# Optimization experiments

Measured on AMD Instinct MI355X. Metric: run time of the kernel, lower is better.

Reference implementation:

```python
import jax, jax.numpy as jnp
import numpy as np
from jax import lax
from jax.scipy.special import logsumexp

B, S, T = 64, 512, 32
END_IND = T - 1  # module-level global in the original repo; bind to last tag


def setup_inputs() -> dict:
    key = jax.random.key(0)
    k1, k2, k3 = jax.random.split(key, 3)
    scores = jax.random.normal(k1, (B, S, T, T), dtype=jnp.float32)
    targets = jax.random.randint(k2, (B, S), 0, T * T, dtype=jnp.int32).astype(jnp.int64)
    # lengths in [1, S], sorted descending (pack_padded_sequence assumption)
    lengths = jnp.sort(jax.random.randint(k3, (B,), 1, S + 1, dtype=jnp.int32))[::-1]
    return {"scores": scores, "targets": targets, "lengths": lengths}


def reference(scores, targets, lengths):
    Bs, Ss, Ts, _ = scores.shape
    # gold score: gather flattened tag-pair score at each valid timestep
    flat = scores.reshape(Bs, Ss, Ts * Ts)
    gathered = jnp.take_along_axis(flat, targets[..., None], axis=2)[..., 0]  # [B,S]
    time_mask = jnp.arange(Ss)[None, :] < lengths[:, None]  # [B,S]
    gold_score = jnp.sum(jnp.where(time_mask, gathered, 0.0))

    # forward algorithm: fs[b, cur_tag], recurrence lse over prev_tag
    fs0 = logsumexp(scores[:, 0], axis=2)  # [B,T]
    sc_rest = jnp.swapaxes(scores, 0, 1)[1:]  # [S-1, B, T, T]
    active = jnp.arange(1, Ss)[:, None] < lengths[None, :]  # [S-1, B]

    def step(fs, xs):
        sc_t, act = xs  # [B,T,T], [B]
        new = logsumexp(sc_t + fs[:, None, :], axis=2)  # [B,T]
        return jnp.where(act[:, None], new, fs), None

    fs, _ = lax.scan(step, fs0, (sc_rest, active))
    all_scores = jnp.sum(fs[:, END_IND])
    return all_scores - gold_score
```

## Files before the change

### kernel.cpp

```cpp
#include <hip/hip_runtime.h>
#include <hip/hip_bf16.h>

#define BB 64
#define SS 512
#define TT 32
#define ENDI 31
#define NSEG 32
#define SEGLEN 16
#define ACCS 0
#define CNTS 1
#define GOLDB 16

typedef __attribute__((ext_vector_type(8))) short s8v;
typedef __attribute__((ext_vector_type(16))) float fx16;

union S8U {
  s8v v;
  unsigned int u[4];
};

__device__ __forceinline__ unsigned int cvtpk_bf16(float a, float b) {
  unsigned int r;
  asm("v_cvt_pk_bf16_f32 %0, %1, %2" : "=v"(r) : "v"(a), "v"(b));
  return r;
}

__global__ __launch_bounds__(64) void seg_kernel(
    const float* __restrict__ sc, const int* __restrict__ targets,
    const int* __restrict__ lengths, float* __restrict__ ws) {
  const int b = blockIdx.x;
  const int seg = blockIdx.y;
  const int l = threadIdx.x;
  const int c = l & 31;
  const int h = l >> 5;
  const int len = lengths[b];
  const int lo = seg * SEGLEN;

  if (b == 0 && seg == 0 && l == 0) {
    ws[ACCS] = 0.0f;
    ((unsigned*)ws)[CNTS] = 0u;
  }

  {
    float gv = 0.f;
    if (l < SEGLEN) {
      int s = lo + l;
      if (s < len) {
        int idx = b * SS + s;
        gv = sc[(size_t)idx * 1024 + (size_t)targets[idx]];
      }
    }
#pragma unroll
    for (int o = 32; o; o >>= 1) gv += __shfl_xor(gv, o);
    if (l == 0) ws[GOLDB + b * NSEG + seg] = gv;
  }

  float* mout = ws + GOLDB + BB * NSEG + (size_t)(b * NSEG + seg) * 1056;

  if (len <= lo) {
#pragma unroll
    for (int r = 0; r < 16; ++r) {
      int row = (r & 3) + 8 * (r >> 2) + 4 * h;
      mout[row * 32 + c] = (row == c) ? 1.0f : 0.0f;
    }
    if (l == 0) mout[1024] = 0.0f;
    return;
  }

  const int nsteps = (len - lo < SEGLEN) ? (len - lo) : SEGLEN;
  const float* base = sc + ((size_t)b * SS + lo) * 1024;

  S8U B0, B1;
#pragma unroll
  for (int q = 0; q < 4; ++q) {
    B0.u[q] = 0u;
    B1.u[q] = 0u;
  }
  {
    int j0 = c - 8 * h;
    if (j0 >= 0 && j0 < 8) B0.u[j0 >> 1] |= 0x3F80u << (16 * (j0 & 1));
    int j1 = c - 16 - 8 * h;
    if (j1 >= 0 && j1 < 8) B1.u[j1 >> 1] |= 0x3F80u << (16 * (j1 & 1));
  }

#define LOADE(buf, T)                                                     \
  do {                                                                    \
    const float* _p = base + (size_t)(T) * 1024 + c * 32 + 8 * h;         \
    float4 _a = *(const float4*)_p;                                       \
    float4 _b = *(const float4*)(_p + 4);                                 \
    float4 _c = *(const float4*)(_p + 16);                                \
    float4 _d = *(const float4*)(_p + 20);                                \
    buf[0] = _a.x;  buf[1] = _a.y;  buf[2] = _a.z;  buf[3] = _a.w;        \
    buf[4] = _b.x;  buf[5] = _b.y;  buf[6] = _b.z;  buf[7] = _b.w;        \
    buf[8] = _c.x;  buf[9] = _c.y;  buf[10] = _c.z; buf[11] = _c.w;       \
    buf[12] = _d.x; buf[13] = _d.y; buf[14] = _d.z; buf[15] = _d.w;       \
  } while (0)

#define RESCALE(SVAR)                                                     \
  do {                                                                    \
    float _mx = Cl[0];                                                    \
    _Pragma("unroll") for (int q = 1; q < 16; ++q) _mx = fmaxf(_mx, Cl[q]); \
    _mx = fmaxf(_mx, __shfl_xor(_mx, 32));                                \
    _mx = fmaxf(_mx, __shfl_xor(_mx, 1));                                 \
    _mx = fmaxf(_mx, __shfl_xor(_mx, 2));                                 \
    _mx = fmaxf(_mx, __shfl_xor(_mx, 4));                                 \
    _mx = fmaxf(_mx, __shfl_xor(_mx, 8));                                 \
    _mx = fmaxf(_mx, __shfl_xor(_mx, 16));                                \
    int _ex = ((__float_as_int(_mx) >> 23) & 255) - 127;                  \
    SVAR = __int_as_float((unsigned)(127 - _ex) << 23);                   \
    esum += _ex;                                                          \
  } while (0)

#define REPACK()                                                          \
  do {                                                                    \
    unsigned int W[8], X[8];                                              \
    _Pragma("unroll") for (int q = 0; q < 8; ++q) W[q] =                  \
        cvtpk_bf16(Cl[2 * q] * s, Cl[2 * q + 1] * s);                     \
    _Pragma("unroll") for (int q = 0; q < 8; ++q) X[q] =                  \
        __shfl_xor((int)W[q], 32);                                        \
    B0.u[0] = h ? X[2] : W[0];                                            \
    B0.u[1] = h ? X[3] : W[1];                                            \
    B0.u[2] = h ? W[2] : X[0];                                            \
    B0.u[3] = h ? W[3] : X[1];                                            \
    B1.u[0] = h ? X[6] : W[4];                                            \
    B1.u[1] = h ? X[7] : W[5];                                            \
    B1.u[2] = h ? W[6] : X[4];                                            \
    B1.u[3] = h ? W[7] : X[5];                                            \
  } while (0)

  int esum = 0;
  fx16 C;
#pragma unroll
  for (int q = 0; q < 16; ++q) C[q] = 0.f;

  if (nsteps == SEGLEN) {
    float L[4][16];
    S8U A4[4][2];
#pragma unroll
    for (int j = 0; j < 4; ++j) LOADE(L[j], j);

#pragma unroll
    for (int ch = 0; ch < 4; ++ch) {
#pragma unroll
      for (int k = 0; k < 4; ++k) {
#pragma unroll
        for (int q = 0; q < 4; ++q) {
          A4[k][0].u[q] =
              cvtpk_bf16(__expf(L[k][2 * q]), __expf(L[k][2 * q + 1]));
          A4[k][1].u[q] =
              cvtpk_bf16(__expf(L[k][8 + 2 * q]), __expf(L[k][9 + 2 * q]));
        }
      }
      if (ch < 3) {
#pragma unroll
        for (int j = 0; j < 4; ++j) LOADE(L[j], (ch + 1) * 4 + j);
      }
#pragma unroll
      for (int k = 0; k < 4; ++k) {
        fx16 Cl;
#pragma unroll
        for (int q = 0; q < 16; ++q) Cl[q] = 0.f;
        Cl = __builtin_amdgcn_mfma_f32_32x32x16_bf16(A4[k][0].v, B0.v, Cl,
                                                     0, 0, 0);
        Cl = __builtin_amdgcn_mfma_f32_32x32x16_bf16(A4[k][1].v, B1.v, Cl,
                                                     0, 0, 0);
        if (ch == 3 && k == 3) {
          C = Cl;
        } else {
          float s = 1.0f;
          if (k == 3) RESCALE(s);
          REPACK();
        }
      }
    }
  } else {
    float r0[16], r1[16], r2[16];
    LOADE(r0, 0);
    LOADE(r1, (nsteps > 1) ? 1 : 0);
    LOADE(r2, (nsteps > 2) ? 2 : 0);

#define STEPB(RB)                                                            \
    do {                                                                    \
      S8U A0, A1;                                                           \
      _Pragma("unroll") for (int q = 0; q < 4; ++q) {                       \
        A0.u[q] = cvtpk_bf16(__expf(RB[2 * q]), __expf(RB[2 * q + 1]));     \
        A1.u[q] = cvtpk_bf16(__expf(RB[8 + 2 * q]), __expf(RB[9 + 2 * q])); \
      }                                                                     \
      int _pf = t + 3;                                                      \
      if (_pf >= nsteps) _pf = nsteps - 1;                                  \
      LOADE(RB, _pf);                                                       \
      fx16 Cl;                                                              \
      _Pragma("unroll") for (int q = 0; q < 16; ++q) Cl[q] = 0.f;           \
      Cl = __builtin_amdgcn_mfma_f32_32x32x16_bf16(A0.v, B0.v, Cl, 0, 0, 0);\
      Cl = __builtin_amdgcn_mfma_f32_32x32x16_bf16(A1.v, B1.v, Cl, 0, 0, 0);\
      if (t + 1 < nsteps) {                                                 \
        float s = 1.0f;                                                     \
        if ((t & 3) == 3) RESCALE(s);                                       \
        REPACK();                                                           \
      } else {                                                              \
        C = Cl;                                                             \
      }                                                                     \
    } while (0)

    int t = 0;
    while (t < nsteps) {
      STEPB(r0);
      ++t;
      if (t >= nsteps) break;
      STEPB(r1);
      ++t;
      if (t >= nsteps) break;
      STEPB(r2);
      ++t;
    }
#undef STEPB
  }

  float mx = C[0];
#pragma unroll
  for (int q = 1; q < 16; ++q) mx = fmaxf(mx, C[q]);
  mx = fmaxf(mx, __shfl_xor(mx, 32));
  mx = fmaxf(mx, __shfl_xor(mx, 1));
  mx = fmaxf(mx, __shfl_xor(mx, 2));
  mx = fmaxf(mx, __shfl_xor(mx, 4));
  mx = fmaxf(mx, __shfl_xor(mx, 8));
  mx = fmaxf(mx, __shfl_xor(mx, 16));
  int ex = ((__float_as_int(mx) >> 23) & 255) - 127;
  float s = __int_as_float((unsigned)(127 - ex) << 23);
  esum += ex;
#pragma unroll
  for (int r = 0; r < 16; ++r) {
    int row = (r & 3) + 8 * (r >> 2) + 4 * h;
    mout[row * 32 + c] = C[r] * s;
  }
  if (l == 0) mout[1024] = (float)esum;
#undef REPACK
#undef RESCALE
#undef LOADE
}

__global__ __launch_bounds__(128) void comb_fin_kernel(
    float* __restrict__ ws, float* __restrict__ out) {
  const int b = blockIdx.x;
  const int w = threadIdx.x >> 6;
  const int l = threadIdx.x & 63;
  const int lo = l & 31;
  const int h = l >> 5;
  const int half = NSEG >> 1;
  __shared__ alignas(16) float st[2][TT];
  __shared__ float esvS[2];

#define FENCE() asm volatile("s_waitcnt lgkmcnt(0)" ::: "memory")

  float cur = w ? ((lo == ENDI) ? 1.0f : 0.0f) : 1.0f;
  st[w][lo] = cur;
  FENCE();

  const float* segbase = ws + GOLDB + BB * NSEG;
  float esv = 0.f;

#define LOADM(buf, SEG)                                                     \
  do {                                                                      \
    const float* _m = segbase + (size_t)(b * NSEG + (SEG)) * 1056;          \
    if (w == 0) {                        \
      const float4* _p = (const float4*)(_m + lo * 32 + h * 16);            \
      float4 _a = _p[0], _b2 = _p[1], _c2 = _p[2], _d = _p[3];              \
      buf[0] = _a.x;  buf[1] = _a.y;  buf[2] = _a.z;  buf[3] = _a.w;        \
      buf[4] = _b2.x; buf[5] = _b2.y; buf[6] = _b2.z; buf[7] = _b2.w;       \
      buf[8] = _c2.x; buf[9] = _c2.y; buf[10] = _c2.z; buf[11] = _c2.w;     \
      buf[12] = _d.x; buf[13] = _d.y; buf[14] = _d.z; buf[15] = _d.w;       \
    } else {      \
      const float* _p = _m + (h * 16) * 32 + lo;                            \
      _Pragma("unroll") for (int _j = 0; _j < 16; ++_j)                     \
          buf[_j] = _p[_j * 32];                                            \
    }                                                                       \
  } while (0)

  float mc[16], mn[16];
#pragma unroll
  for (int q = 0; q < 16; ++q) mn[q] = 0.f;
  {
    int seg0 = w ? (NSEG - 1) : 0;
    LOADM(mc, seg0);
  }
  for (int k = 0; k < half; ++k) {
    int segn = w ? (NSEG - 2 - k) : (k + 1);
    if (k + 1 < half) LOADM(mn, segn);
    int segc = w ? (NSEG - 1 - k) : k;
    esv += segbase[(size_t)(b * NSEG + segc) * 1056 + 1024];
    const float4* g4 = (const float4*)st[w];
    float4 g0 = g4[h * 4 + 0], g1 = g4[h * 4 + 1], g2 = g4[h * 4 + 2],
           g3 = g4[h * 4 + 3];
    float g[16] = {g0.x, g0.y, g0.z, g0.w, g1.x, g1.y, g1.z, g1.w,
                   g2.x, g2.y, g2.z, g2.w, g3.x, g3.y, g3.z, g3.w};
    float acc[4];
#pragma unroll
    for (int q = 0; q < 4; ++q) {
      acc[q] = mc[4 * q] * g[4 * q];
#pragma unroll
      for (int t = 1; t < 4; ++t)
        acc[q] = fmaf(mc[4 * q + t], g[4 * q + t], acc[q]);
    }
    float part = (acc[0] + acc[1]) + (acc[2] + acc[3]);
    cur = part + __shfl_xor(part, 32);
    if ((k & 3) == 3) {
      float mxv = cur;
      mxv = fmaxf(mxv, __shfl_xor(mxv, 1));
      mxv = fmaxf(mxv, __shfl_xor(mxv, 2));
      mxv = fmaxf(mxv, __shfl_xor(mxv, 4));
      mxv = fmaxf(mxv, __shfl_xor(mxv, 8));
      mxv = fmaxf(mxv, __shfl_xor(mxv, 16));
      int exv = ((__float_as_int(mxv) >> 23) & 255) - 127;
      cur *= __int_as_float((unsigned)(127 - exv) << 23);
      esv += (float)exv;
    }
    FENCE();
    st[w][lo] = cur;
    FENCE();
#pragma unroll
    for (int q = 0; q < 16; ++q) mc[q] = mn[q];
  }

  if (l == 0) esvS[w] = esv;
  __syncthreads();

  if (w == 0) {
    float pr = st[0][lo] * st[1][lo];
    float gd = ws[GOLDB + b * NSEG + lo];
#pragma unroll
    for (int o = 16; o; o >>= 1) {
      pr += __shfl_xor(pr, o);
      gd += __shfl_xor(gd, o);
    }
    if (l == 0) {
      float loss =
          (esvS[0] + esvS[1]) * 0.6931471805599453f + __logf(pr) - gd;
      atomicAdd(&ws[ACCS], loss);
      __threadfence();
      unsigned old = atomicAdd(&((unsigned*)ws)[CNTS], 1u);
      if (old == BB - 1) {
        float v = atomicAdd(&ws[ACCS], 0.0f);
        out[0] = v;
      }
    }
  }
#undef LOADM
#undef FENCE
}

extern "C" void kernel_launch(void* const* d_in, const int* in_sizes, int n_in,
                              void* d_out, int out_size, void* d_ws,
                              size_t ws_size, hipStream_t stream) {
  const float* scores = (const float*)d_in[0];
  const int* targets = (const int*)d_in[1];
  const int* lengths = (const int*)d_in[2];
  float* out = (float*)d_out;
  float* ws = (float*)d_ws;

  seg_kernel<<<dim3(BB, NSEG), 64, 0, stream>>>(scores, targets, lengths, ws);
  comb_fin_kernel<<<BB, 128, 0, stream>>>(ws, out);
}
```

Before: 49.79 us.

## Split each segment's chain across two waves and merge via LDS matmul

Each seg_kernel block now runs two wavefronts, and each one computes the product chain for half of a 16-step segment (8 steps each). The second wave normalizes its partial matrix and writes it to shared memory. The first wave then multiplies it in with one extra MFMA pair before writing out. This shortens the serial dependency chain per block and doubles the wave count, at the cost of a __syncthreads, LDS traffic, and one extra bf16 rounding in the merge.

```diff
diff --git a/kernel.cpp b/kernel.cpp
--- a/kernel.cpp
+++ b/kernel.cpp
@@ -7,6 +7,7 @@
 #define ENDI 31
 #define NSEG 32
 #define SEGLEN 16
+#define HALF 8
 #define ACCS 0
 #define CNTS 1
 #define GOLDB 16
@@ -25,23 +26,28 @@
   return r;
 }
 
-__global__ __launch_bounds__(64) void seg_kernel(
+__global__ __launch_bounds__(128) void seg_kernel(
     const float* __restrict__ sc, const int* __restrict__ targets,
     const int* __restrict__ lengths, float* __restrict__ ws) {
   const int b = blockIdx.x;
   const int seg = blockIdx.y;
-  const int l = threadIdx.x;
+  const int tid = threadIdx.x;
+  const int wv = tid >> 6;
+  const int l = tid & 63;
   const int c = l & 31;
   const int h = l >> 5;
   const int len = lengths[b];
   const int lo = seg * SEGLEN;
 
-  if (b == 0 && seg == 0 && l == 0) {
+  __shared__ alignas(16) float lm[TT * 33];
+  __shared__ float meta0;
+
+  if (b == 0 && seg == 0 && tid == 0) {
     ws[ACCS] = 0.0f;
     ((unsigned*)ws)[CNTS] = 0u;
   }
 
-  {
+  if (wv == 0) {
     float gv = 0.f;
     if (l < SEGLEN) {
       int s = lo + l;
@@ -58,17 +64,23 @@
   float* mout = ws + GOLDB + BB * NSEG + (size_t)(b * NSEG + seg) * 1056;
 
   if (len <= lo) {
-#pragma unroll
-    for (int r = 0; r < 16; ++r) {
-      int row = (r & 3) + 8 * (r >> 2) + 4 * h;
-      mout[row * 32 + c] = (row == c) ? 1.0f : 0.0f;
-    }
-    if (l == 0) mout[1024] = 0.0f;
+    if (wv == 0) {
+#pragma unroll
+      for (int r = 0; r < 16; ++r) {
+        int row = (r & 3) + 8 * (r >> 2) + 4 * h;
+        mout[row * 32 + c] = (row == c) ? 1.0f : 0.0f;
+      }
+      if (l == 0) mout[1024] = 0.0f;
+    }
     return;
   }
 
-  const int nsteps = (len - lo < SEGLEN) ? (len - lo) : SEGLEN;
-  const float* base = sc + ((size_t)b * SS + lo) * 1024;
+  const int rel = len - lo;
+  const int nst = (wv == 0) ? (rel < HALF ? rel : HALF)
+                            : (rel - HALF < 0 ? 0
+                                              : (rel - HALF < HALF ? rel - HALF
+                                                                   : HALF));
+  const float* base = sc + ((size_t)b * SS + lo + wv * HALF) * 1024;
 
   S8U B0, B1;
 #pragma unroll
@@ -133,51 +145,51 @@
 #pragma unroll
   for (int q = 0; q < 16; ++q) C[q] = 0.f;
 
-  if (nsteps == SEGLEN) {
-    float L[4][16];
-    S8U A4[4][2];
-#pragma unroll
-    for (int j = 0; j < 4; ++j) LOADE(L[j], j);
-
-#pragma unroll
-    for (int ch = 0; ch < 4; ++ch) {
-#pragma unroll
-      for (int k = 0; k < 4; ++k) {
+  if (nst == HALF) {
+    float L[2][16];
+    S8U A2[2][2];
+    LOADE(L[0], 0);
+    LOADE(L[1], 1);
+#pragma unroll
+    for (int ph = 0; ph < 4; ++ph) {
+#pragma unroll
+      for (int k = 0; k < 2; ++k) {
 #pragma unroll
         for (int q = 0; q < 4; ++q) {
-          A4[k][0].u[q] =
+          A2[k][0].u[q] =
               cvtpk_bf16(__expf(L[k][2 * q]), __expf(L[k][2 * q + 1]));
-          A4[k][1].u[q] =
+          A2[k][1].u[q] =
               cvtpk_bf16(__expf(L[k][8 + 2 * q]), __expf(L[k][9 + 2 * q]));
         }
       }
-      if (ch < 3) {
-#pragma unroll
-        for (int j = 0; j < 4; ++j) LOADE(L[j], (ch + 1) * 4 + j);
-      }
-#pragma unroll
-      for (int k = 0; k < 4; ++k) {
+      if (ph < 3) {
+        LOADE(L[0], ph * 2 + 2);
+        LOADE(L[1], ph * 2 + 3);
+      }
+#pragma unroll
+      for (int k = 0; k < 2; ++k) {
+        const int t = ph * 2 + k;
         fx16 Cl;
 #pragma unroll
         for (int q = 0; q < 16; ++q) Cl[q] = 0.f;
-        Cl = __builtin_amdgcn_mfma_f32_32x32x16_bf16(A4[k][0].v, B0.v, Cl,
+        Cl = __builtin_amdgcn_mfma_f32_32x32x16_bf16(A2[k][0].v, B0.v, Cl,
                                                      0, 0, 0);
-        Cl = __builtin_amdgcn_mfma_f32_32x32x16_bf16(A4[k][1].v, B1.v, Cl,
+        Cl = __builtin_amdgcn_mfma_f32_32x32x16_bf16(A2[k][1].v, B1.v, Cl,
                                                      0, 0, 0);
-        if (ch == 3 && k == 3) {
+        if (t == HALF - 1) {
           C = Cl;
         } else {
           float s = 1.0f;
-          if (k == 3) RESCALE(s);
+          if (t == 3) RESCALE(s);
           REPACK();
         }
       }
     }
-  } else {
+  } else if (nst > 0) {
     float r0[16], r1[16], r2[16];
     LOADE(r0, 0);
-    LOADE(r1, (nsteps > 1) ? 1 : 0);
-    LOADE(r2, (nsteps > 2) ? 2 : 0);
+    LOADE(r1, (nst > 1) ? 1 : 0);
+    LOADE(r2, (nst > 2) ? 2 : 0);
 
 #define STEPB(RB)                                                            \
     do {                                                                    \
@@ -187,13 +199,13 @@
         A1.u[q] = cvtpk_bf16(__expf(RB[8 + 2 * q]), __expf(RB[9 + 2 * q])); \
       }                                                                     \
       int _pf = t + 3;                                                      \
-      if (_pf >= nsteps) _pf = nsteps - 1;                                  \
+      if (_pf >= nst) _pf = nst - 1;                                        \
       LOADE(RB, _pf);                                                       \
       fx16 Cl;                                                              \
       _Pragma("unroll") for (int q = 0; q < 16; ++q) Cl[q] = 0.f;           \
       Cl = __builtin_amdgcn_mfma_f32_32x32x16_bf16(A0.v, B0.v, Cl, 0, 0, 0);\
       Cl = __builtin_amdgcn_mfma_f32_32x32x16_bf16(A1.v, B1.v, Cl, 0, 0, 0);\
-      if (t + 1 < nsteps) {                                                 \
+      if (t + 1 < nst) {                                                    \
         float s = 1.0f;                                                     \
         if ((t & 3) == 3) RESCALE(s);                                       \
         REPACK();                                                           \
@@ -203,37 +215,84 @@
     } while (0)
 
     int t = 0;
-    while (t < nsteps) {
+    while (t < nst) {
       STEPB(r0);
       ++t;
-      if (t >= nsteps) break;
+      if (t >= nst) break;
       STEPB(r1);
       ++t;
-      if (t >= nsteps) break;
+      if (t >= nst) break;
       STEPB(r2);
       ++t;
     }
 #undef STEPB
   }
 
-  float mx = C[0];
-#pragma unroll
-  for (int q = 1; q < 16; ++q) mx = fmaxf(mx, C[q]);
-  mx = fmaxf(mx, __shfl_xor(mx, 32));
-  mx = fmaxf(mx, __shfl_xor(mx, 1));
-  mx = fmaxf(mx, __shfl_xor(mx, 2));
-  mx = fmaxf(mx, __shfl_xor(mx, 4));
-  mx = fmaxf(mx, __shfl_xor(mx, 8));
-  mx = fmaxf(mx, __shfl_xor(mx, 16));
-  int ex = ((__float_as_int(mx) >> 23) & 255) - 127;
-  float s = __int_as_float((unsigned)(127 - ex) << 23);
-  esum += ex;
-#pragma unroll
-  for (int r = 0; r < 16; ++r) {
-    int row = (r & 3) + 8 * (r >> 2) + 4 * h;
-    mout[row * 32 + c] = C[r] * s;
-  }
-  if (l == 0) mout[1024] = (float)esum;
+  if (wv == 1 && nst > 0) {
+    float mx = C[0];
+#pragma unroll
+    for (int q = 1; q < 16; ++q) mx = fmaxf(mx, C[q]);
+    mx = fmaxf(mx, __shfl_xor(mx, 32));
+    mx = fmaxf(mx, __shfl_xor(mx, 1));
+    mx = fmaxf(mx, __shfl_xor(mx, 2));
+    mx = fmaxf(mx, __shfl_xor(mx, 4));
+    mx = fmaxf(mx, __shfl_xor(mx, 8));
+    mx = fmaxf(mx, __shfl_xor(mx, 16));
+    int ex = ((__float_as_int(mx) >> 23) & 255) - 127;
+    float s1 = __int_as_float((unsigned)(127 - ex) << 23);
+    esum += ex;
+#pragma unroll
+    for (int r = 0; r < 16; ++r) {
+      int row = (r & 3) + 8 * (r >> 2) + 4 * h;
+      lm[row * 33 + c] = C[r] * s1;
+    }
+    if (l == 0) meta0 = (float)esum;
+  }
+  __syncthreads();
+
+  if (wv == 0) {
+    if (rel > HALF) {
+      {
+        fx16 Cl = C;
+        float s = 1.0f;
+        RESCALE(s);
+        REPACK();
+      }
+      S8U Am0, Am1;
+#pragma unroll
+      for (int q = 0; q < 4; ++q) {
+        Am0.u[q] = cvtpk_bf16(lm[c * 33 + 8 * h + 2 * q],
+                              lm[c * 33 + 8 * h + 2 * q + 1]);
+        Am1.u[q] = cvtpk_bf16(lm[c * 33 + 16 + 8 * h + 2 * q],
+                              lm[c * 33 + 16 + 8 * h + 2 * q + 1]);
+      }
+      fx16 Cm;
+#pragma unroll
+      for (int q = 0; q < 16; ++q) Cm[q] = 0.f;
+      Cm = __builtin_amdgcn_mfma_f32_32x32x16_bf16(Am0.v, B0.v, Cm, 0, 0, 0);
+      Cm = __builtin_amdgcn_mfma_f32_32x32x16_bf16(Am1.v, B1.v, Cm, 0, 0, 0);
+      C = Cm;
+      esum += (int)meta0;
+    }
+    float mx = C[0];
+#pragma unroll
+    for (int q = 1; q < 16; ++q) mx = fmaxf(mx, C[q]);
+    mx = fmaxf(mx, __shfl_xor(mx, 32));
+    mx = fmaxf(mx, __shfl_xor(mx, 1));
+    mx = fmaxf(mx, __shfl_xor(mx, 2));
+    mx = fmaxf(mx, __shfl_xor(mx, 4));
+    mx = fmaxf(mx, __shfl_xor(mx, 8));
+    mx = fmaxf(mx, __shfl_xor(mx, 16));
+    int ex = ((__float_as_int(mx) >> 23) & 255) - 127;
+    float s = __int_as_float((unsigned)(127 - ex) << 23);
+    esum += ex;
+#pragma unroll
+    for (int r = 0; r < 16; ++r) {
+      int row = (r & 3) + 8 * (r >> 2) + 4 * h;
+      mout[row * 32 + c] = C[r] * s;
+    }
+    if (l == 0) mout[1024] = (float)esum;
+  }
 #undef REPACK
 #undef RESCALE
 #undef LOADE
@@ -262,14 +321,14 @@
 #define LOADM(buf, SEG)                                                     \
   do {                                                                      \
     const float* _m = segbase + (size_t)(b * NSEG + (SEG)) * 1056;          \
-    if (w == 0) {                        \
+    if (w == 0) {                                                           \
       const float4* _p = (const float4*)(_m + lo * 32 + h * 16);            \
       float4 _a = _p[0], _b2 = _p[1], _c2 = _p[2], _d = _p[3];              \
       buf[0] = _a.x;  buf[1] = _a.y;  buf[2] = _a.z;  buf[3] = _a.w;        \
       buf[4] = _b2.x; buf[5] = _b2.y; buf[6] = _b2.z; buf[7] = _b2.w;       \
       buf[8] = _c2.x; buf[9] = _c2.y; buf[10] = _c2.z; buf[11] = _c2.w;     \
       buf[12] = _d.x; buf[13] = _d.y; buf[14] = _d.z; buf[15] = _d.w;       \
-    } else {      \
+    } else {                                                                \
       const float* _p = _m + (h * 16) * 32 + lo;                            \
       _Pragma("unroll") for (int _j = 0; _j < 16; ++_j)                     \
           buf[_j] = _p[_j * 32];                                            \
@@ -357,6 +416,6 @@
   float* out = (float*)d_out;
   float* ws = (float*)d_ws;
 
-  seg_kernel<<<dim3(BB, NSEG), 64, 0, stream>>>(scores, targets, lengths, ws);
+  seg_kernel<<<dim3(BB, NSEG), 128, 0, stream>>>(scores, targets, lengths, ws);
   comb_fin_kernel<<<BB, 128, 0, stream>>>(ws, out);
 }
```

Measured after the change: 47.17 us. -5.3%, faster.
